# Performance work log

Hardware: AMD Instinct MI355X
Metric: run time of the kernel (lower is better)

Reference implementation:

```python
import jax, jax.numpy as jnp
import numpy as np

B = 2048   # jets (graphs)
P = 50     # particles per jet
N = B * P  # nodes
E = B * P * P  # within-jet all-pairs radius-graph edges (incl. self-loops)
H = 5      # edge-MLP width ([5,5,5,5] channel list)
EPS = 1e-5
NEG_SLOPE = 0.01


def _batchnorm(h, gamma, beta):
    # training-mode batch norm over the edge dimension (biased variance, as torch)
    mu = jnp.mean(h, axis=0)
    var = jnp.mean(h * h, axis=0) - mu * mu
    return gamma * (h - mu) * jax.lax.rsqrt(var + EPS) + beta


def setup_inputs() -> dict:
    key = jax.random.key(0)
    ks = jax.random.split(key, 16)
    # angles: per-jet center offset + tight spread so all within-jet pairs are inside dR=0.4
    centers = jax.random.normal(ks[0], (B, 1, 2), dtype=jnp.float32) + jnp.array([2.0, 0.5], dtype=jnp.float32)
    angles = (centers + 0.1 * jax.random.normal(ks[1], (B, P, 2), dtype=jnp.float32)).reshape(N, 2)
    pt = jax.random.uniform(ks[2], (N,), dtype=jnp.float32, minval=0.1, maxval=1.0)
    features = jnp.linalg.norm(angles, axis=-1, keepdims=True)  # rho = |view_as_complex(angles)|, [N,1]
    # radius graph: with the tight spread every within-jet pair is within dR -> fixed E
    ii = np.arange(P)
    pi, pj = np.meshgrid(ii, ii, indexing='ij')
    base = (np.arange(B, dtype=np.int64) * P)[:, None]
    src = (base + pj.ravel()[None, :]).ravel()  # x_j (source)
    dst = (base + pi.ravel()[None, :]).ravel()  # x_i (target) = aggregation index
    edge_index = jnp.asarray(np.stack([src, dst]), dtype=jnp.int32)  # [2, E]
    def lin(k, o, i):
        return (jax.random.normal(k, (o, i), dtype=jnp.float32) / np.sqrt(i)).astype(jnp.float32)
    W1 = lin(ks[3], H, 5); b1 = jnp.zeros((H,), jnp.float32)
    W2 = lin(ks[4], H, H); b2 = jnp.zeros((H,), jnp.float32)
    W3 = lin(ks[5], H, H); b3 = jnp.zeros((H,), jnp.float32)
    g1 = jnp.ones((H,), jnp.float32); bt1 = jnp.zeros((H,), jnp.float32)
    g2 = jnp.ones((H,), jnp.float32); bt2 = jnp.zeros((H,), jnp.float32)
    return {"pt": pt, "features": features, "angles": angles,
            "W1": W1, "b1": b1, "g1": g1, "bt1": bt1,
            "W2": W2, "b2": b2, "g2": g2, "bt2": bt2,
            "W3": W3, "b3": b3, "edge_index": edge_index}


def reference(pt, features, angles, W1, b1, g1, bt1, W2, b2, g2, bt2, W3, b3, edge_index):
    src = edge_index[0]  # j (source)
    dst = edge_index[1]  # i (target, aggregation index)
    x = jnp.concatenate([pt[:, None], features, angles], axis=1)  # [N, 4]
    xi = x[dst]  # [E, 4]
    xj = x[src]
    # complex ratio angles_i / angles_j in real arithmetic
    ar, ai = xi[:, 2], xi[:, 3]
    br, bi = xj[:, 2], xj[:, 3]
    den = br * br + bi * bi
    dr = (ar * br + ai * bi) / den
    di = (ai * br - ar * bi) / den
    fi = xi[:, 1:2]
    fj = xj[:, 1:2]
    mlp_in = jnp.concatenate([fi, fj, fj - fi, dr[:, None], di[:, None]], axis=1)  # [E, 5]
    h = jax.nn.leaky_relu(_batchnorm(mlp_in @ W1.T + b1, g1, bt1), NEG_SLOPE)
    h = jax.nn.leaky_relu(_batchnorm(h @ W2.T + b2, g2, bt2), NEG_SLOPE)
    h = h @ W3.T + b3  # [E, 5]
    msg = jnp.concatenate([xi[:, :1], h, xi[:, 2:4]], axis=1)  # [E, 8]
    pt_e = msg[:, 0]
    denom = jax.ops.segment_sum(pt_e, dst, num_segments=N)  # [N]
    wj = pt_e / denom[dst]
    agg = jax.ops.segment_sum(wj[:, None] * msg, dst, num_segments=N)  # [N, 8]
    # exp(2*pi*i*theta) * z with theta = agg[:, -3], z = complex(agg[:, -2:])
    theta = agg[:, 5]
    zr, zi = agg[:, 6], agg[:, 7]
    c = jnp.cos(2.0 * jnp.pi * theta)
    s = jnp.sin(2.0 * jnp.pi * theta)
    out = jnp.concatenate([agg[:, :5], (c * zr - s * zi)[:, None], (c * zi + s * zr)[:, None]], axis=1)  # [N, 7]
    return out
```

## Files before the change

### kernel.cpp

```cpp
#include <hip/hip_runtime.h>

#define PP 50
#define TPB 256
#define NBATCH 2048
#define GB 2
#define NBLK2 (NBATCH / GB)
#define NBLK1 512
#define NCOPY 32

static constexpr float EPSF = 1e-5f;
static constexpr double INV_ETOT = 1.0 / 5120000.0;

static __device__ __forceinline__ float lrelu(float x) {
    return fmaxf(x, 0.01f * x);
}
static __device__ __forceinline__ float rfl(float x) {
    return __int_as_float(__builtin_amdgcn_readfirstlane(__float_as_int(x)));
}

__global__ __launch_bounds__(TPB) void stats1_kernel(
    const float* __restrict__ feat, const float* __restrict__ ang,
    const float* __restrict__ W1, const float* __restrict__ b1,
    double* __restrict__ acc, double* __restrict__ pacc)
{
    __shared__ double bacc[4][10];
    const int t = threadIdx.x;
    const int lane = t & 63;
    const int wv = t >> 6;

    if (blockIdx.x == 0) {
        for (int i = t; i < 20 * NCOPY; i += TPB) acc[i] = 0.0;
    }

    float v0[5], v1[5], v2[5], v3[5], bb1[5];
#pragma unroll
    for (int o = 0; o < 5; ++o) {
        v0[o] = rfl(W1[o*5+0] - W1[o*5+2]);
        v1[o] = rfl(W1[o*5+1] + W1[o*5+2]);
        v2[o] = rfl(W1[o*5+3]);
        v3[o] = rfl(W1[o*5+4]);
        bb1[o] = rfl(b1[o]);
    }

    float f = 0.f, zr = 0.f, zi = 0.f, inv = 0.f;
    if (lane < PP) {
        const int idx = (blockIdx.x * 4 + wv) * PP + lane;
        f = feat[idx];
        float2 a2 = ((const float2*)ang)[idx];
        zr = a2.x; zi = a2.y;
        inv = 1.0f / (zr*zr + zi*zi);
    }
    const float wr = zr * inv, wi = -zi * inv;

    float p[16] = { f, f*f, zr, zi, wr, wi, f*zr, f*zi, f*wr, f*wi,
                    zr*zr, zi*zi, zr*zi, wr*wr, wi*wi, wr*wi };
#pragma unroll
    for (int k = 0; k < 16; ++k) {
        float v = p[k];
#pragma unroll
        for (int off = 32; off > 0; off >>= 1) v += __shfl_down(v, off, 64);
        p[k] = v;
    }
    if (lane == 0) {
        const double P0 = p[0], P1 = p[1], P2 = p[2], P3 = p[3], P4 = p[4];
        const double P5 = p[5], P6 = p[6], P7 = p[7], P8 = p[8], P9 = p[9];
        const double P10 = p[10], P11 = p[11], P12 = p[12];
        const double P13 = p[13], P14 = p[14], P15 = p[15];
        const double Sfi = 50.0 * P0;
        const double Sdr = P2*P4 - P3*P5;
        const double Sdi = P3*P4 + P2*P5;
        const double m00 = 50.0 * P1, m11 = m00, m01 = P0*P0;
        const double m02 = P6*P4 - P7*P5;
        const double m03 = P7*P4 + P6*P5;
        const double m12 = P2*P8 - P3*P9;
        const double m13 = P3*P8 + P2*P9;
        const double m22 = P10*P13 - 2.0*P12*P15 + P11*P14;
        const double m33 = P11*P13 + 2.0*P12*P15 + P10*P14;
        const double m23 = P12*P13 + P10*P15 - P11*P15 - P12*P14;
#pragma unroll
        for (int o = 0; o < 5; ++o) {
            const double a0=v0[o], a1=v1[o], a2=v2[o], a3=v3[o], bo=bb1[o];
            const double sy = a0*Sfi + a1*Sfi + a2*Sdr + a3*Sdi + 2500.0*bo;
            const double q  = a0*a0*m00 + a1*a1*m11 + a2*a2*m22 + a3*a3*m33
                           + 2.0*(a0*a1*m01 + a0*a2*m02 + a0*a3*m03
                                + a1*a2*m12 + a1*a3*m13 + a2*a3*m23);
            bacc[wv][o]   = sy;
            bacc[wv][5+o] = q + 2.0*bo*sy - 2500.0*bo*bo;
        }
    }
    __syncthreads();
    if (t < 10) {
        pacc[t * NBLK1 + blockIdx.x] =
            bacc[0][t] + bacc[1][t] + bacc[2][t] + bacc[3][t];
    }
}

__global__ __launch_bounds__(TPB, 2) void pass2_kernel(
    const float* __restrict__ feat, const float* __restrict__ ang,
    const float* __restrict__ W1, const float* __restrict__ b1,
    const float* __restrict__ g1, const float* __restrict__ bt1,
    double* __restrict__ acc, const double* __restrict__ pacc)
{
    __shared__ float4 nd[GB * PP];
    __shared__ float4 ndj[GB * PP];
    __shared__ double tmp[10];
    __shared__ double pred[10][16];
    __shared__ float red[4][20];
    const int t = threadIdx.x;

    if (t < GB * PP) {
        const int idx = blockIdx.x * (GB * PP) + t;
        float f = feat[idx];
        float2 a2 = ((const float2*)ang)[idx];
        float inv = 1.0f / (a2.x*a2.x + a2.y*a2.y);
        nd[t]  = make_float4(f, a2.x, a2.y, 0.0f);
        ndj[t] = make_float4(f, a2.x * inv, a2.y * inv, 0.0f);
    } else if (t >= 100 && t < 250) {
        const int r = t - 100;
        const int slot = r / 15, sub = r - slot * 15;
        double s = 0.0;
        for (int b = sub; b < NBLK1; b += 15) s += pacc[slot * NBLK1 + b];
        pred[slot][sub] = s;
    }

    float v0[5], v1[5], v2[5], v3[5], bb1[5];
#pragma unroll
    for (int o = 0; o < 5; ++o) {
        v0[o] = rfl(W1[o*5+0] - W1[o*5+2]);
        v1[o] = rfl(W1[o*5+1] + W1[o*5+2]);
        v2[o] = rfl(W1[o*5+3]);
        v3[o] = rfl(W1[o*5+4]);
        bb1[o] = rfl(b1[o]);
    }

    __syncthreads();
    if (t < 10) {
        double s = 0.0;
#pragma unroll
        for (int k = 0; k < 15; ++k) s += pred[t][k];
        tmp[t] = s;
    }
    __syncthreads();

#pragma unroll
    for (int o = 0; o < 5; ++o) {
        double mu  = tmp[o]   * INV_ETOT;
        double var = tmp[5+o] * INV_ETOT - mu * mu;
        float sc = rfl(g1[o]) * rsqrtf((float)var + EPSF);
        float sh = rfl(rfl(bt1[o]) - (float)mu * sc);
        v0[o] = rfl(v0[o] * sc);
        v1[o] = rfl(v1[o] * sc);
        v2[o] = rfl(v2[o] * sc);
        v3[o] = rfl(v3[o] * sc);
        bb1[o] = rfl(fmaf(bb1[o], sc, sh));
    }

    float s1[5] = {0.f, 0.f, 0.f, 0.f, 0.f};
    float mm[15];
#pragma unroll
    for (int k = 0; k < 15; ++k) mm[k] = 0.f;

    if (t < 250) {
        const int pi = t / 5;
        const int s5 = t - pi*5;
#pragma unroll
        for (int g = 0; g < GB; ++g) {
            const float4 ni = nd[g*PP + pi];
            const float fi = ni.x, ari = ni.y, aii = ni.z;
            float4 njs[10];
#pragma unroll
            for (int q = 0; q < 10; ++q) njs[q] = ndj[g*PP + s5*10 + q];
#pragma unroll
            for (int q = 0; q < 10; ++q) {
                const float4 nj = njs[q];
                const float dr = fmaf(ari, nj.y,  aii*nj.z);
                const float di = fmaf(aii, nj.y, -ari*nj.z);
                float h1[5];
#pragma unroll
                for (int o = 0; o < 5; ++o) {
                    float y = fmaf(v0[o], fi, fmaf(v1[o], nj.x,
                              fmaf(v2[o], dr, fmaf(v3[o], di, bb1[o]))));
                    h1[o] = lrelu(y);
                }
#pragma unroll
                for (int k = 0; k < 5; ++k) {
                    s1[k] += h1[k];
#pragma unroll
                    for (int l = k; l < 5; ++l) {
                        const int idx = k*5 - (k*(k+1))/2 + l;
                        mm[idx] = fmaf(h1[k], h1[l], mm[idx]);
                    }
                }
            }
        }
    }

    float a[20];
#pragma unroll
    for (int k = 0; k < 5; ++k) a[k] = s1[k];
#pragma unroll
    for (int k = 0; k < 15; ++k) a[5+k] = mm[k];
#pragma unroll
    for (int k = 0; k < 20; ++k) {
        float v = a[k];
#pragma unroll
        for (int off = 32; off > 0; off >>= 1) v += __shfl_down(v, off, 64);
        a[k] = v;
    }
    const int lane = t & 63, wv = t >> 6;
    if (lane == 0) {
#pragma unroll
        for (int k = 0; k < 20; ++k) red[wv][k] = a[k];
    }
    __syncthreads();
    if (t < 20) {
        atomicAdd(&acc[t * NCOPY + (blockIdx.x & (NCOPY-1))],
                  (double)(red[0][t] + red[1][t] + red[2][t] + red[3][t]));
    }
}

__global__ __launch_bounds__(TPB, 2) void pass3_kernel(
    const float* __restrict__ pt,
    const float* __restrict__ feat, const float* __restrict__ ang,
    const float* __restrict__ W1, const float* __restrict__ b1,
    const float* __restrict__ g1, const float* __restrict__ bt1,
    const float* __restrict__ W2, const float* __restrict__ b2,
    const float* __restrict__ g2, const float* __restrict__ bt2,
    const float* __restrict__ W3, const float* __restrict__ b3,
    const double* __restrict__ acc, const double* __restrict__ pacc,
    float* __restrict__ out)
{
    __shared__ float4 nd[GB * PP];
    __shared__ float4 ndj[GB * PP];
    __shared__ float spt[GB * PP];
    __shared__ double tmp[30];
    __shared__ double pred[10][16];
    __shared__ float scsh[2][5];
    __shared__ float part[250][5];
    __shared__ __align__(16) float ob[PP * 7 + 2];
    const int t = threadIdx.x;

    if (t < GB * PP) {
        const int idx = blockIdx.x * (GB * PP) + t;
        float f = feat[idx];
        float2 a2 = ((const float2*)ang)[idx];
        float inv = 1.0f / (a2.x*a2.x + a2.y*a2.y);
        nd[t]  = make_float4(f, a2.x, a2.y, 0.0f);
        ndj[t] = make_float4(f, a2.x * inv, a2.y * inv, 0.0f);
        spt[t] = pt[idx];
    }
    if (t < 20) {
        double s = 0.0;
#pragma unroll
        for (int c = 0; c < NCOPY; ++c) s += acc[t * NCOPY + c];
        tmp[10 + t] = s;
    } else if (t >= 100 && t < 250) {
        const int r = t - 100;
        const int slot = r / 15, sub = r - slot * 15;
        double s = 0.0;
        for (int b = sub; b < NBLK1; b += 15) s += pacc[slot * NBLK1 + b];
        pred[slot][sub] = s;
    }

    float v0[5], v1[5], v2[5], v3[5], bb1[5], w2[25], bb2[5], w3[25], bb3[5];
#pragma unroll
    for (int o = 0; o < 5; ++o) {
        v0[o] = rfl(W1[o*5+0] - W1[o*5+2]);
        v1[o] = rfl(W1[o*5+1] + W1[o*5+2]);
        v2[o] = rfl(W1[o*5+3]);
        v3[o] = rfl(W1[o*5+4]);
        bb1[o] = rfl(b1[o]); bb2[o] = rfl(b2[o]); bb3[o] = rfl(b3[o]);
    }
#pragma unroll
    for (int i = 0; i < 25; ++i) { w2[i] = rfl(W2[i]); w3[i] = rfl(W3[i]); }

    __syncthreads();
    if (t < 10) {
        double s = 0.0;
#pragma unroll
        for (int k = 0; k < 15; ++k) s += pred[t][k];
        tmp[t] = s;
    }
    __syncthreads();

#pragma unroll
    for (int o = 0; o < 5; ++o) {
        double mu  = tmp[o]   * INV_ETOT;
        double var = tmp[5+o] * INV_ETOT - mu * mu;
        float sc = rfl(g1[o]) * rsqrtf((float)var + EPSF);
        float sh = rfl(rfl(bt1[o]) - (float)mu * sc);
        v0[o] = rfl(v0[o] * sc);
        v1[o] = rfl(v1[o] * sc);
        v2[o] = rfl(v2[o] * sc);
        v3[o] = rfl(v3[o] * sc);
        bb1[o] = rfl(fmaf(bb1[o], sc, sh));
    }

    if (t < 5) {
        const int o = t;
        double w[5], Sn[5];
#pragma unroll
        for (int k = 0; k < 5; ++k) {
            w[k]  = (double)w2[o*5+k];
            Sn[k] = tmp[10+k] * INV_ETOT;
        }
        double muw = 0.0;
#pragma unroll
        for (int k = 0; k < 5; ++k) muw += w[k] * Sn[k];
        double q = 0.0;
#pragma unroll
        for (int k = 0; k < 5; ++k) {
#pragma unroll
            for (int l = k; l < 5; ++l) {
                const int idx = k*5 - (k*(k+1))/2 + l;
                const double Mn = tmp[15+idx] * INV_ETOT;
                q += (k == l ? w[k]*w[k] : 2.0*w[k]*w[l]) * Mn;
            }
        }
        double var2 = q - muw * muw;
        double mu2  = muw + (double)bb2[o];
        float sc2 = g2[o] * rsqrtf((float)var2 + EPSF);
        scsh[0][o] = sc2;
        scsh[1][o] = bt2[o] - (float)mu2 * sc2;
    }
    __syncthreads();

#pragma unroll
    for (int o = 0; o < 5; ++o) {
        const float s2f = rfl(scsh[0][o]);
        const float s2h = rfl(scsh[1][o]);
#pragma unroll
        for (int k = 0; k < 5; ++k) w2[o*5+k] = rfl(w2[o*5+k] * s2f);
        bb2[o] = rfl(fmaf(bb2[o], s2f, s2h));
    }

    const int pi = t / 5;
    const int s5 = t - pi*5;

#pragma unroll
    for (int g = 0; g < GB; ++g) {
        float a[5] = {0.f, 0.f, 0.f, 0.f, 0.f};
        if (t < 250) {
            const float4 ni = nd[g*PP + pi];
            const float fi = ni.x, ari = ni.y, aii = ni.z;
            float4 njs[10];
#pragma unroll
            for (int q = 0; q < 10; ++q) njs[q] = ndj[g*PP + s5*10 + q];
#pragma unroll
            for (int q = 0; q < 10; ++q) {
                const float4 nj = njs[q];
                const float dr = fmaf(ari, nj.y,  aii*nj.z);
                const float di = fmaf(aii, nj.y, -ari*nj.z);
                float h1[5], h2[5];
#pragma unroll
                for (int o = 0; o < 5; ++o) {
                    float y = fmaf(v0[o], fi, fmaf(v1[o], nj.x,
                              fmaf(v2[o], dr, fmaf(v3[o], di, bb1[o]))));
                    h1[o] = lrelu(y);
                }
#pragma unroll
                for (int o = 0; o < 5; ++o) {
                    float y = bb2[o];
                    y = fmaf(w2[o*5+0], h1[0], y);
                    y = fmaf(w2[o*5+1], h1[1], y);
                    y = fmaf(w2[o*5+2], h1[2], y);
                    y = fmaf(w2[o*5+3], h1[3], y);
                    y = fmaf(w2[o*5+4], h1[4], y);
                    h2[o] = lrelu(y);
                }
#pragma unroll
                for (int o = 0; o < 5; ++o) a[o] += h2[o];
            }
#pragma unroll
            for (int c = 0; c < 5; ++c) part[t][c] = a[c];
        }
        __syncthreads();

        if (t < PP) {
            float hm[5];
#pragma unroll
            for (int c = 0; c < 5; ++c) {
                hm[c] = (part[5*t][c] + part[5*t+1][c] + part[5*t+2][c] +
                         part[5*t+3][c] + part[5*t+4][c]) * 0.02f;
            }
            float m[5];
#pragma unroll
            for (int c = 0; c < 5; ++c) {
                float y = bb3[c];
                y = fmaf(w3[c*5+0], hm[0], y);
                y = fmaf(w3[c*5+1], hm[1], y);
                y = fmaf(w3[c*5+2], hm[2], y);
                y = fmaf(w3[c*5+3], hm[3], y);
                y = fmaf(w3[c*5+4], hm[4], y);
                m[c] = y;
            }
            const int node = g*PP + t;
            const float4 ni = nd[node];
            float ss, cc;
            sincosf(6.2831853071795865f * m[4], &ss, &cc);
            float* o = &ob[t * 7];
            o[0] = spt[node];
            o[1] = m[0];
            o[2] = m[1];
            o[3] = m[2];
            o[4] = m[3];
            o[5] = cc * ni.y - ss * ni.z;
            o[6] = cc * ni.z + ss * ni.y;
        }
        __syncthreads();

        if (t < 175) {
            float2* dst = (float2*)(out +
                (size_t)(blockIdx.x * (GB * PP) + g * PP) * 7);
            dst[t] = ((const float2*)ob)[t];
        }
        __syncthreads();
    }
}

extern "C" void kernel_launch(void* const* d_in, const int* in_sizes, int n_in,
                              void* d_out, int out_size, void* d_ws, size_t ws_size,
                              hipStream_t stream)
{
    const float* pt   = (const float*)d_in[0];
    const float* feat = (const float*)d_in[1];
    const float* ang  = (const float*)d_in[2];
    const float* W1   = (const float*)d_in[3];
    const float* b1   = (const float*)d_in[4];
    const float* g1   = (const float*)d_in[5];
    const float* bt1  = (const float*)d_in[6];
    const float* W2   = (const float*)d_in[7];
    const float* b2   = (const float*)d_in[8];
    const float* g2   = (const float*)d_in[9];
    const float* bt2  = (const float*)d_in[10];
    const float* W3   = (const float*)d_in[11];
    const float* b3   = (const float*)d_in[12];
    float* out = (float*)d_out;
    double* acc  = (double*)d_ws;
    double* pacc = acc + 20 * NCOPY;

    stats1_kernel<<<NBLK1, TPB, 0, stream>>>(feat, ang, W1, b1, acc, pacc);
    pass2_kernel<<<NBLK2, TPB, 0, stream>>>(feat, ang, W1, b1, g1, bt1, acc, pacc);
    pass3_kernel<<<NBLK2, TPB, 0, stream>>>(pt, feat, ang, W1, b1, g1, bt1,
                                            W2, b2, g2, bt2, W3, b3,
                                            acc, pacc, out);
}
```

Baseline: 152.2 us.

## Use 1024-thread blocks processing 8 jets in parallel across four sub-groups

Block size grows from 256 to 1024 threads. The edge passes now run four independent 250-thread groups, each handling two jets, so a block covers 8 jets and the block count drops by 4x. The stats kernel processes 16 jets per block, which shrinks the per-block partial-sum array, and the pacc reduction in the later passes becomes a fixed 32-way tree. The aim is to use the previously idle threads (only 250 of 256 were busy) and amortise per-block setup work (weight loads, BN reduction) over more jets. In exchange, each block uses more shared memory and registers, and the larger blocks may lower occupancy.

After: 138.1 us. -9.3%, faster.

```diff
diff --git a/kernel.cpp b/kernel.cpp
--- a/kernel.cpp
+++ b/kernel.cpp
@@ -1,11 +1,12 @@
 #include <hip/hip_runtime.h>
 
 #define PP 50
-#define TPB 256
+#define TPB 1024
 #define NBATCH 2048
-#define GB 2
+#define GBK 16
+#define NBLK1 (NBATCH / GBK)
+#define GB 8
 #define NBLK2 (NBATCH / GB)
-#define NBLK1 512
 #define NCOPY 32
 
 static constexpr float EPSF = 1e-5f;
@@ -23,14 +24,12 @@
     const float* __restrict__ W1, const float* __restrict__ b1,
     double* __restrict__ acc, double* __restrict__ pacc)
 {
-    __shared__ double bacc[4][10];
+    __shared__ double bacc[GBK][10];
     const int t = threadIdx.x;
     const int lane = t & 63;
     const int wv = t >> 6;
 
-    if (blockIdx.x == 0) {
-        for (int i = t; i < 20 * NCOPY; i += TPB) acc[i] = 0.0;
-    }
+    if (blockIdx.x == 0 && t < 20 * NCOPY) acc[t] = 0.0;
 
     float v0[5], v1[5], v2[5], v3[5], bb1[5];
 #pragma unroll
@@ -44,7 +43,7 @@
 
     float f = 0.f, zr = 0.f, zi = 0.f, inv = 0.f;
     if (lane < PP) {
-        const int idx = (blockIdx.x * 4 + wv) * PP + lane;
+        const int idx = (blockIdx.x * GBK + wv) * PP + lane;
         f = feat[idx];
         float2 a2 = ((const float2*)ang)[idx];
         zr = a2.x; zi = a2.y;
@@ -90,12 +89,14 @@
     }
     __syncthreads();
     if (t < 10) {
-        pacc[t * NBLK1 + blockIdx.x] =
-            bacc[0][t] + bacc[1][t] + bacc[2][t] + bacc[3][t];
-    }
-}
-
-__global__ __launch_bounds__(TPB, 2) void pass2_kernel(
+        double s = 0.0;
+#pragma unroll
+        for (int w = 0; w < GBK; ++w) s += bacc[w][t];
+        pacc[t * NBLK1 + blockIdx.x] = s;
+    }
+}
+
+__global__ __launch_bounds__(TPB) void pass2_kernel(
     const float* __restrict__ feat, const float* __restrict__ ang,
     const float* __restrict__ W1, const float* __restrict__ b1,
     const float* __restrict__ g1, const float* __restrict__ bt1,
@@ -103,9 +104,9 @@
 {
     __shared__ float4 nd[GB * PP];
     __shared__ float4 ndj[GB * PP];
+    __shared__ double predl[10][32];
     __shared__ double tmp[10];
-    __shared__ double pred[10][16];
-    __shared__ float red[4][20];
+    __shared__ float red[16][20];
     const int t = threadIdx.x;
 
     if (t < GB * PP) {
@@ -115,12 +116,11 @@
         float inv = 1.0f / (a2.x*a2.x + a2.y*a2.y);
         nd[t]  = make_float4(f, a2.x, a2.y, 0.0f);
         ndj[t] = make_float4(f, a2.x * inv, a2.y * inv, 0.0f);
-    } else if (t >= 100 && t < 250) {
-        const int r = t - 100;
-        const int slot = r / 15, sub = r - slot * 15;
-        double s = 0.0;
-        for (int b = sub; b < NBLK1; b += 15) s += pacc[slot * NBLK1 + b];
-        pred[slot][sub] = s;
+    } else if (t >= 512 && t < 832) {
+        const int r = t - 512;
+        const int slot = r >> 5, sub = r & 31;
+        const double* pp = &pacc[slot * NBLK1];
+        predl[slot][sub] = pp[sub] + pp[sub+32] + pp[sub+64] + pp[sub+96];
     }
 
     float v0[5], v1[5], v2[5], v3[5], bb1[5];
@@ -137,7 +137,7 @@
     if (t < 10) {
         double s = 0.0;
 #pragma unroll
-        for (int k = 0; k < 15; ++k) s += pred[t][k];
+        for (int k = 0; k < 32; ++k) s += predl[t][k];
         tmp[t] = s;
     }
     __syncthreads();
@@ -155,21 +155,25 @@
         bb1[o] = rfl(fmaf(bb1[o], sc, sh));
     }
 
+    const int p  = t / 250;
+    const int r  = t - p * 250;
+    const int pi = r / 5;
+    const int s5 = r - pi * 5;
+
     float s1[5] = {0.f, 0.f, 0.f, 0.f, 0.f};
     float mm[15];
 #pragma unroll
     for (int k = 0; k < 15; ++k) mm[k] = 0.f;
 
-    if (t < 250) {
-        const int pi = t / 5;
-        const int s5 = t - pi*5;
-#pragma unroll
-        for (int g = 0; g < GB; ++g) {
-            const float4 ni = nd[g*PP + pi];
+    if (t < 1000) {
+#pragma unroll
+        for (int g = 0; g < 2; ++g) {
+            const int b = p * 2 + g;
+            const float4 ni = nd[b*PP + pi];
             const float fi = ni.x, ari = ni.y, aii = ni.z;
             float4 njs[10];
 #pragma unroll
-            for (int q = 0; q < 10; ++q) njs[q] = ndj[g*PP + s5*10 + q];
+            for (int q = 0; q < 10; ++q) njs[q] = ndj[b*PP + s5*10 + q];
 #pragma unroll
             for (int q = 0; q < 10; ++q) {
                 const float4 nj = njs[q];
@@ -214,12 +218,14 @@
     }
     __syncthreads();
     if (t < 20) {
-        atomicAdd(&acc[t * NCOPY + (blockIdx.x & (NCOPY-1))],
-                  (double)(red[0][t] + red[1][t] + red[2][t] + red[3][t]));
-    }
-}
-
-__global__ __launch_bounds__(TPB, 2) void pass3_kernel(
+        float s = 0.f;
+#pragma unroll
+        for (int w = 0; w < 16; ++w) s += red[w][t];
+        atomicAdd(&acc[t * NCOPY + (blockIdx.x & (NCOPY-1))], (double)s);
+    }
+}
+
+__global__ __launch_bounds__(TPB) void pass3_kernel(
     const float* __restrict__ pt,
     const float* __restrict__ feat, const float* __restrict__ ang,
     const float* __restrict__ W1, const float* __restrict__ b1,
@@ -233,11 +239,11 @@
     __shared__ float4 nd[GB * PP];
     __shared__ float4 ndj[GB * PP];
     __shared__ float spt[GB * PP];
+    __shared__ double predl[10][32];
     __shared__ double tmp[30];
-    __shared__ double pred[10][16];
     __shared__ float scsh[2][5];
-    __shared__ float part[250][5];
-    __shared__ __align__(16) float ob[PP * 7 + 2];
+    __shared__ float part[1000][5];
+    __shared__ __align__(16) float ob[4 * 350];
     const int t = threadIdx.x;
 
     if (t < GB * PP) {
@@ -248,18 +254,17 @@
         nd[t]  = make_float4(f, a2.x, a2.y, 0.0f);
         ndj[t] = make_float4(f, a2.x * inv, a2.y * inv, 0.0f);
         spt[t] = pt[idx];
-    }
-    if (t < 20) {
+    } else if (t >= 512 && t < 832) {
+        const int r = t - 512;
+        const int slot = r >> 5, sub = r & 31;
+        const double* pp = &pacc[slot * NBLK1];
+        predl[slot][sub] = pp[sub] + pp[sub+32] + pp[sub+64] + pp[sub+96];
+    } else if (t >= 832 && t < 852) {
+        const int k = t - 832;
         double s = 0.0;
 #pragma unroll
-        for (int c = 0; c < NCOPY; ++c) s += acc[t * NCOPY + c];
-        tmp[10 + t] = s;
-    } else if (t >= 100 && t < 250) {
-        const int r = t - 100;
-        const int slot = r / 15, sub = r - slot * 15;
-        double s = 0.0;
-        for (int b = sub; b < NBLK1; b += 15) s += pacc[slot * NBLK1 + b];
-        pred[slot][sub] = s;
+        for (int c = 0; c < NCOPY; ++c) s += acc[k * NCOPY + c];
+        tmp[10 + k] = s;
     }
 
     float v0[5], v1[5], v2[5], v3[5], bb1[5], w2[25], bb2[5], w3[25], bb3[5];
@@ -278,7 +283,7 @@
     if (t < 10) {
         double s = 0.0;
 #pragma unroll
-        for (int k = 0; k < 15; ++k) s += pred[t][k];
+        for (int k = 0; k < 32; ++k) s += predl[t][k];
         tmp[t] = s;
     }
     __syncthreads();
@@ -334,18 +339,21 @@
         bb2[o] = rfl(fmaf(bb2[o], s2f, s2h));
     }
 
-    const int pi = t / 5;
-    const int s5 = t - pi*5;
-
-#pragma unroll
-    for (int g = 0; g < GB; ++g) {
+    const int p  = t / 250;
+    const int r  = t - p * 250;
+    const int pi = r / 5;
+    const int s5 = r - pi * 5;
+
+#pragma unroll
+    for (int g = 0; g < 2; ++g) {
         float a[5] = {0.f, 0.f, 0.f, 0.f, 0.f};
-        if (t < 250) {
-            const float4 ni = nd[g*PP + pi];
+        if (t < 1000) {
+            const int b = p * 2 + g;
+            const float4 ni = nd[b*PP + pi];
             const float fi = ni.x, ari = ni.y, aii = ni.z;
             float4 njs[10];
 #pragma unroll
-            for (int q = 0; q < 10; ++q) njs[q] = ndj[g*PP + s5*10 + q];
+            for (int q = 0; q < 10; ++q) njs[q] = ndj[b*PP + s5*10 + q];
 #pragma unroll
             for (int q = 0; q < 10; ++q) {
                 const float4 nj = njs[q];
@@ -376,12 +384,13 @@
         }
         __syncthreads();
 
-        if (t < PP) {
+        if (t < 1000 && r < PP) {
             float hm[5];
 #pragma unroll
             for (int c = 0; c < 5; ++c) {
-                hm[c] = (part[5*t][c] + part[5*t+1][c] + part[5*t+2][c] +
-                         part[5*t+3][c] + part[5*t+4][c]) * 0.02f;
+                const int base = p * 250 + 5 * r;
+                hm[c] = (part[base][c] + part[base+1][c] + part[base+2][c] +
+                         part[base+3][c] + part[base+4][c]) * 0.02f;
             }
             float m[5];
 #pragma unroll
@@ -394,11 +403,12 @@
                 y = fmaf(w3[c*5+4], hm[4], y);
                 m[c] = y;
             }
-            const int node = g*PP + t;
+            const int b = p * 2 + g;
+            const int node = b * PP + r;
             const float4 ni = nd[node];
             float ss, cc;
             sincosf(6.2831853071795865f * m[4], &ss, &cc);
-            float* o = &ob[t * 7];
+            float* o = &ob[p * 350 + r * 7];
             o[0] = spt[node];
             o[1] = m[0];
             o[2] = m[1];
@@ -409,10 +419,11 @@
         }
         __syncthreads();
 
-        if (t < 175) {
-            float2* dst = (float2*)(out +
-                (size_t)(blockIdx.x * (GB * PP) + g * PP) * 7);
-            dst[t] = ((const float2*)ob)[t];
+        if (t < 700) {
+            const int pp = t / 175, k = t - pp * 175;
+            float2* dst = (float2*)(out + (size_t)blockIdx.x * (GB * PP * 7)
+                                        + (size_t)(pp * 2 + g) * 350);
+            dst[k] = ((const float2*)ob)[pp * 175 + k];
         }
         __syncthreads();
     }
```
